# Performance work log

Measured on AMD Instinct MI355X. Metric: run time of the kernel, lower is better.

The kernel has to match this reference:

```python
import jax, jax.numpy as jnp
import numpy as np

N, M, E, H = 4096, 16384, 512, 8
D = E // H  # head dim = 64


def _rms(x, g, eps=1e-6):
    return x * jax.lax.rsqrt(jnp.mean(jnp.square(x), axis=-1, keepdims=True) + eps) * g


def _split(x):
    # (rows, E) -> (rows, H, D)
    return x.reshape(x.shape[0], H, D)


def _sdpa(q, k, v):
    # Faithful to the source layout: SDPA on (rows, H, D) tensors, i.e. per-row
    # attention over the H heads (tiny HxH softmax per node).
    s = jnp.einsum('nhd,ngd->nhg', q, k) / jnp.sqrt(jnp.asarray(D, q.dtype))
    a = jax.nn.softmax(s, axis=-1)
    return jnp.einsum('nhg,ngd->nhd', a, v).reshape(-1, E)


def setup_inputs() -> dict:
    key = jax.random.key(0)
    ks = jax.random.split(key, 25)
    w = lambda k, s, sc: jax.random.normal(k, s, dtype=jnp.float32) * sc
    se = 1.0 / np.sqrt(E)   # Linear(E, E) init scale
    sm = 1.0 / np.sqrt(M)   # Linear(M, N) init scale
    inp = {
        'x_node': jax.random.normal(ks[0], (N, E), dtype=jnp.float32),
        'x_edge': jax.random.normal(ks[1], (M, E), dtype=jnp.float32),
        # sparse-ish binary adjacency, avg degree ~8
        'adj': (jax.random.uniform(ks[2], (N, N)) < 0.002).astype(jnp.float32),
        # per-branch QKV weights (4 separate MultiHeadAttention modules)
        'Wq_hh': w(ks[3], (E, E), se), 'Wk_hh': w(ks[4], (E, E), se), 'Wv_hh': w(ks[5], (E, E), se),
        'Wq_ee': w(ks[6], (E, E), se), 'Wk_ee': w(ks[7], (E, E), se), 'Wv_ee': w(ks[8], (E, E), se),
        'Wq_he': w(ks[9], (E, E), se), 'Wk_he': w(ks[10], (E, E), se), 'Wv_he': w(ks[11], (E, E), se),
        'Wq_eh': w(ks[12], (E, E), se), 'Wk_eh': w(ks[13], (E, E), se), 'Wv_eh': w(ks[14], (E, E), se),
        # shape_proj (edges -> nodes) weights, one per module that uses it
        'Wp1_he': w(ks[15], (N, M), sm),
        'Wp1_eh': w(ks[16], (N, M), sm),
        'Wp1_ee': w(ks[17], (N, M), sm),
        # RMSNorm gains
        'g_n': jnp.ones((E,), jnp.float32),
        'g_e': jnp.ones((E,), jnp.float32),
        'g2': jnp.ones((E,), jnp.float32),
        # FeedForward
        'Wf1': w(ks[18], (E, 4 * E), se), 'bf1': jnp.zeros((4 * E,), jnp.float32),
        'Wf2': w(ks[19], (4 * E, E), 1.0 / np.sqrt(4 * E)), 'bf2': jnp.zeros((E,), jnp.float32),
    }
    return inp


def reference(x_node, x_edge, adj,
              Wq_hh, Wk_hh, Wv_hh, Wq_ee, Wk_ee, Wv_ee,
              Wq_he, Wk_he, Wv_he, Wq_eh, Wk_eh, Wv_eh,
              Wp1_he, Wp1_eh, Wp1_ee,
              g_n, g_e, g2, Wf1, bf1, Wf2, bf2):
    h = _rms(x_node, g_n)   # (N, E)
    e = _rms(x_edge, g_e)   # (M, E)

    # hh: adjacency injected into the node query branch
    q = jnp.einsum('nm,mhd->nhd', adj, _split(h @ Wq_hh))
    out_hh = _sdpa(q, _split(h @ Wk_hh), _split(h @ Wv_hh))

    # ee: edge queries/keys projected to node rows via shape_proj
    q = jnp.einsum('nm,mhd->nhd', Wp1_ee, _split(e @ Wq_ee))
    k = jnp.einsum('nm,mhd->nhd', Wp1_ee, _split(e @ Wk_ee))
    out_ee = _sdpa(q, k, _split(h @ Wv_ee))

    # eh: edge query projected to node rows, node key
    q = jnp.einsum('nm,mhd->nhd', Wp1_eh, _split(e @ Wq_eh))
    out_eh = _sdpa(q, _split(h @ Wk_eh), _split(h @ Wv_eh))

    # he: node query, edge key projected to node rows
    k = jnp.einsum('nm,mhd->nhd', Wp1_he, _split(e @ Wk_he))
    out_he = _sdpa(_split(h @ Wq_he), k, _split(h @ Wv_he))

    x = out_hh + out_ee + out_eh + out_he          # (N, E)
    y = _rms(x, g2)
    return jax.nn.gelu(y @ Wf1 + bf1, approximate=False) @ Wf2 + bf2
```

## Files before the change

### kernel.cpp

```cpp
#include <hip/hip_runtime.h>
#include <cstdint>


typedef unsigned short u16;
typedef __bf16 bf16x8 __attribute__((ext_vector_type(8)));
typedef float f32x4 __attribute__((ext_vector_type(4)));

__device__ __forceinline__ u16 f2bf(float f) {
    unsigned u = __float_as_uint(f);
    return (u16)((u + 0x7fffu + ((u >> 16) & 1u)) >> 16);
}
__device__ __forceinline__ float bf2f(u16 u) { return __uint_as_float(((unsigned)u) << 16); }
__device__ __forceinline__ float gelu_exact(float x) {
    return 0.5f * x * (1.0f + erff(x * 0.70710678118654752f));
}

__device__ __forceinline__ void gload_lds16(const void* g, void* l) {
    __builtin_amdgcn_global_load_lds(
        (const __attribute__((address_space(1))) unsigned int*)(uintptr_t)g,
        (__attribute__((address_space(3))) unsigned int*)(unsigned int)(uintptr_t)l,
        16, 0, 0);
}

__device__ __forceinline__ void swz_block(int& bx, int& by, int& bz) {
    const int nx = gridDim.x, ny = gridDim.y;
    const int nwg = nx * ny * gridDim.z;
    int lin = blockIdx.x + nx * (blockIdx.y + ny * blockIdx.z);
    const int chunk = nwg >> 3;
    lin = (lin & 7) * chunk + (lin >> 3);
    bx = lin % nx;
    lin /= nx;
    by = lin % ny;
    bz = lin / ny;
}

template <bool SWZ>
__global__ __launch_bounds__(256) void cvt_f32_bf16(const float* __restrict__ in,
                                                    u16* __restrict__ out, size_t n8) {
    size_t i = (size_t)blockIdx.x * 256 + threadIdx.x;
    size_t stride = (size_t)gridDim.x * 256;
    for (; i < n8; i += stride) {
        float4 a = ((const float4*)in)[i * 2];
        float4 b = ((const float4*)in)[i * 2 + 1];
        u16 r[8] = {f2bf(a.x), f2bf(a.y), f2bf(a.z), f2bf(a.w),
                    f2bf(b.x), f2bf(b.y), f2bf(b.z), f2bf(b.w)};
        size_t o = i;
        if constexpr (SWZ) o = (i & ~(size_t)63) | ((i & 63) ^ ((i >> 7) & 3));
        ((uint4*)out)[o] = *(const uint4*)r;
    }
}

__global__ __launch_bounds__(256) void transpose_cvt(const float* __restrict__ in,
                                                     u16* __restrict__ out, int R, int C) {
    __shared__ float tile[32][33];
    int c0 = blockIdx.x * 32, r0 = blockIdx.y * 32;
    int tx = threadIdx.x & 31, ty = threadIdx.x >> 5;
#pragma unroll
    for (int i = 0; i < 4; ++i)
        tile[ty + i * 8][tx] = in[(size_t)(r0 + ty + i * 8) * C + c0 + tx];
    __syncthreads();
#pragma unroll
    for (int i = 0; i < 4; ++i) {
        int orow = c0 + ty + i * 8;
        out[(size_t)orow * R + ((r0 + tx) ^ (((orow >> 1) & 3) << 3))] = f2bf(tile[tx][ty + i * 8]);
    }
}

struct W12 { const float* in[12]; u16* out[12]; };
__global__ __launch_bounds__(256) void transpose_cvt12(W12 w) {
    __shared__ float tile[32][33];
    const float* in = w.in[blockIdx.z];
    u16* out = w.out[blockIdx.z];
    int c0 = blockIdx.x * 32, r0 = blockIdx.y * 32;
    int tx = threadIdx.x & 31, ty = threadIdx.x >> 5;
#pragma unroll
    for (int i = 0; i < 4; ++i)
        tile[ty + i * 8][tx] = in[(size_t)(r0 + ty + i * 8) * 512 + c0 + tx];
    __syncthreads();
#pragma unroll
    for (int i = 0; i < 4; ++i) {
        int orow = c0 + ty + i * 8;
        out[(size_t)orow * 512 + ((r0 + tx) ^ (((orow >> 1) & 3) << 3))] = f2bf(tile[tx][ty + i * 8]);
    }
}

__global__ __launch_bounds__(256) void transpose_u16(const u16* __restrict__ in,
                                                     u16* __restrict__ out, int R, int C) {
    __shared__ u16 tile[32][34];
    int c0 = blockIdx.x * 32, r0 = blockIdx.y * 32;
    int tx = threadIdx.x & 31, ty = threadIdx.x >> 5;
#pragma unroll
    for (int i = 0; i < 4; ++i)
        tile[ty + i * 8][tx] = in[(size_t)(r0 + ty + i * 8) * C + c0 + tx];
    __syncthreads();
#pragma unroll
    for (int i = 0; i < 4; ++i) {
        int orow = c0 + ty + i * 8;
        out[(size_t)orow * R + ((r0 + tx) ^ (((orow >> 1) & 3) << 3))] = tile[tx][ty + i * 8];
    }
}

template <bool SWZ>
__global__ __launch_bounds__(256) void rmsnorm_bf16(const float* __restrict__ x,
                                                    const float* __restrict__ g,
                                                    u16* __restrict__ out) {
    int row = blockIdx.x, tid = threadIdx.x;
    const float* xr = x + (size_t)row * 512;
    float2 v = *(const float2*)(xr + tid * 2);
    float ss = v.x * v.x + v.y * v.y;
#pragma unroll
    for (int o = 32; o; o >>= 1) ss += __shfl_down(ss, o);
    __shared__ float red[4];
    if ((tid & 63) == 0) red[tid >> 6] = ss;
    __syncthreads();
    float tot = red[0] + red[1] + red[2] + red[3];
    float rs = rsqrtf(tot * (1.0f / 512.0f) + 1e-6f);
    unsigned pack = (unsigned)f2bf(v.x * rs * g[tid * 2]) |
                    ((unsigned)f2bf(v.y * rs * g[tid * 2 + 1]) << 16);
    int o32 = SWZ ? (tid ^ (((row >> 1) & 3) << 2)) : tid;
    ((unsigned*)out)[(size_t)row * 256 + o32] = pack;
}

__global__ __launch_bounds__(256) void adj_spmm(const float* __restrict__ adj,
                                                const u16* __restrict__ h,
                                                u16* __restrict__ out) {
    const int wave = threadIdx.x >> 6, lane = threadIdx.x & 63;
    const int n = blockIdx.x * 4 + wave;
    const float* arow = adj + (size_t)n * 4096;
    float acc[8] = {0.f, 0.f, 0.f, 0.f, 0.f, 0.f, 0.f, 0.f};
    for (int j = 0; j < 64; ++j) {
        float v = arow[j * 64 + lane];
        unsigned long long mask = __ballot(v != 0.0f);
        while (mask) {
            int bit = __ffsll((long long)mask) - 1;
            mask &= mask - 1;
            int m = j * 64 + bit;
            float w = __shfl(v, bit);
            int cs = (lane & ~3) | ((lane & 3) ^ ((m >> 1) & 3));
            uint4 q = *(const uint4*)(h + (size_t)m * 512 + cs * 8);
            const u16* qu = (const u16*)&q;
#pragma unroll
            for (int t = 0; t < 8; ++t) acc[t] += w * bf2f(qu[t]);
        }
    }
    int co = (lane & ~3) | ((lane & 3) ^ ((n >> 1) & 3));
    u16 r[8];
#pragma unroll
    for (int t = 0; t < 8; ++t) r[t] = f2bf(acc[t]);
    *(uint4*)(out + (size_t)n * 512 + co * 8) = *(const uint4*)r;
}

template <int MODE>
__device__ __forceinline__ void gemm_tile_body(const u16* __restrict__ A,
                                               const u16* __restrict__ Bt,
                                               int N, int K, int k_begin, int k_end,
                                               int rowStart, int colStart,
                                               void* __restrict__ C,
                                               const float* __restrict__ bias) {
    __shared__ u16 Asm[128 * 32];
    __shared__ u16 Bsm[128 * 32];
    const int tid = threadIdx.x;
    const int wave = tid >> 6, lane = tid & 63;
    const int wr = wave >> 1, wc = wave & 1;

    f32x4 acc[4][4];
#pragma unroll
    for (int m = 0; m < 4; ++m)
#pragma unroll
        for (int n = 0; n < 4; ++n) acc[m][n] = f32x4{0.f, 0.f, 0.f, 0.f};

    const int off0 = (wave * 2 + 0) * 1024 + lane * 16;
    const int off1 = (wave * 2 + 1) * 1024 + lane * 16;
    const int r0 = off0 >> 6, k0e = (off0 & 63) >> 1;
    const int r1 = off1 >> 6, k1e = (off1 & 63) >> 1;
    const size_t Arow0 = (size_t)(rowStart + r0) * K + k0e;
    const size_t Arow1 = (size_t)(rowStart + r1) * K + k1e;
    const size_t Brow0 = (size_t)(colStart + r0) * K + k0e;
    const size_t Brow1 = (size_t)(colStart + r1) * K + k1e;
    u16* As0 = &Asm[(wave * 2 + 0) * 512];
    u16* As1 = &Asm[(wave * 2 + 1) * 512];
    u16* Bs0 = &Bsm[(wave * 2 + 0) * 512];
    u16* Bs1 = &Bsm[(wave * 2 + 1) * 512];

    const int rsel = lane & 15, ksel = lane >> 4;
    const int fsw = (ksel ^ ((rsel >> 1) & 3)) << 3;

    for (int kk = k_begin; kk < k_end; kk += 32) {
        gload_lds16(A + Arow0 + kk, As0);
        gload_lds16(A + Arow1 + kk, As1);
        gload_lds16(Bt + Brow0 + kk, Bs0);
        gload_lds16(Bt + Brow1 + kk, Bs1);
        __syncthreads();
        bf16x8 aF[4], bF[4];
#pragma unroll
        for (int m = 0; m < 4; ++m)
            aF[m] = *(const bf16x8*)&Asm[(wr * 64 + m * 16 + rsel) * 32 + fsw];
#pragma unroll
        for (int n = 0; n < 4; ++n)
            bF[n] = *(const bf16x8*)&Bsm[(wc * 64 + n * 16 + rsel) * 32 + fsw];
#pragma unroll
        for (int m = 0; m < 4; ++m)
#pragma unroll
            for (int n = 0; n < 4; ++n)
                acc[m][n] = __builtin_amdgcn_mfma_f32_16x16x32_bf16(aF[m], bF[n], acc[m][n], 0, 0, 0);
        __syncthreads();
    }

    const int cq = (lane >> 4) * 4, cr = lane & 15;
#pragma unroll
    for (int m = 0; m < 4; ++m) {
#pragma unroll
        for (int n = 0; n < 4; ++n) {
            int col = colStart + wc * 64 + n * 16 + cr;
#pragma unroll
            for (int j = 0; j < 4; ++j) {
                int row = rowStart + wr * 64 + m * 16 + cq + j;
                float v = acc[m][n][j];
                if constexpr (MODE == 0) {
                    ((u16*)C)[(size_t)row * N + col] = f2bf(v);
                } else if constexpr (MODE == 1) {
                    v = gelu_exact(v + bias[col]);
                    ((u16*)C)[(size_t)row * N + (col ^ (((row >> 1) & 3) << 3))] = f2bf(v);
                } else {
                    if (bias) v += bias[col];
                    atomicAdd(&((float*)C)[(size_t)row * N + col], v);
                }
            }
        }
    }
}

template <int MODE>
__global__ __launch_bounds__(256) void gemm_bt(const u16* __restrict__ A,
                                               const u16* __restrict__ Bt,
                                               void* __restrict__ C,
                                               const float* __restrict__ bias,
                                               int N, int K, int kLen) {
    int bx, by, bz;
    swz_block(bx, by, bz);
    const float* bb = (MODE == 3) ? ((bz == 0) ? bias : nullptr) : bias;
    int kb = bz * kLen;
    gemm_tile_body<MODE>(A, Bt, N, K, kb, kb + kLen, by * 128, bx * 128, C, bb);
}

struct Small12 { const u16* A[12]; const u16* W[12]; u16* C[12]; };
__global__ __launch_bounds__(256) void gemm_small12(Small12 s) {
    int bx, by, bz;
    swz_block(bx, by, bz);
    gemm_tile_body<0>(s.A[bz], s.W[bz], 512, 512, 0, 512, by * 128, bx * 128, s.C[bz], nullptr);
}

struct Big3 { const float* A[3]; };
__global__ __launch_bounds__(256, 2) void gemm_f32a(Big3 ba, const u16* __restrict__ Bt,
                                                    float* __restrict__ C0, int K,
                                                    int zPerMat, int kLen) {
    __shared__ float Afs[2][4096];
    __shared__ u16 Bsm[2][4096];
    int bx, by, bz;
    swz_block(bx, by, bz);
    const int mat = bz / zPerMat, ks = bz - mat * zPerMat;
    const float* __restrict__ A = ba.A[mat];
    float* __restrict__ C = C0 + (size_t)mat * (4096 * 512);
    const int rowStart = by * 128, colStart = bx * 128;
    const int k0 = ks * kLen;

    const int tid = threadIdx.x;
    const int wave = tid >> 6, lane = tid & 63;
    const int wr = wave >> 1, wc = wave & 1;

    f32x4 acc[4][4];
#pragma unroll
    for (int mm = 0; mm < 4; ++mm)
#pragma unroll
        for (int n = 0; n < 4; ++n) acc[mm][n] = f32x4{0.f, 0.f, 0.f, 0.f};

    const int lrow = lane >> 3;
    const int slot = (lane & 7) ^ lrow;
    size_t asrc[4];
    int adst[4];
#pragma unroll
    for (int i = 0; i < 4; ++i) {
        int row = wave * 32 + i * 8 + lrow;
        asrc[i] = (size_t)(rowStart + row) * K + slot * 4;
        adst[i] = (wave * 4 + i) * 256 + lane * 4;
    }

    const int off0 = (wave * 2 + 0) * 1024 + lane * 16;
    const int off1 = (wave * 2 + 1) * 1024 + lane * 16;
    const int br0 = off0 >> 6, bk0 = (off0 & 63) >> 1;
    const int br1 = off1 >> 6, bk1 = (off1 & 63) >> 1;
    const u16* Bp0 = Bt + (size_t)(colStart + br0) * K + bk0;
    const u16* Bp1 = Bt + (size_t)(colStart + br1) * K + bk1;
    const int ws0 = (wave * 2 + 0) * 512, ws1 = (wave * 2 + 1) * 512;

    const int rsel = lane & 15, ksel = lane >> 4;
    const int fsw = (ksel ^ ((rsel >> 1) & 3)) << 3;

    auto STAGE = [&](int buf, int kk) {
#pragma unroll
        for (int i = 0; i < 4; ++i)
            gload_lds16(A + asrc[i] + kk, &Afs[buf][adst[i]]);
        gload_lds16(Bp0 + kk, &Bsm[buf][ws0]);
        gload_lds16(Bp1 + kk, &Bsm[buf][ws1]);
    };
    auto COMPUTE = [&](int buf) {
        bf16x8 aF[4], bF[4];
#pragma unroll
        for (int mm = 0; mm < 4; ++mm) {
            int R = wr * 64 + mm * 16 + rsel;
            const char* rb = (const char*)&Afs[buf][0] + R * 128;
            f32x4 lo = *(const f32x4*)(rb + ((((ksel << 1) | 0) ^ (R & 7)) << 4));
            f32x4 hi = *(const f32x4*)(rb + ((((ksel << 1) | 1) ^ (R & 7)) << 4));
            aF[mm][0] = (__bf16)lo[0]; aF[mm][1] = (__bf16)lo[1];
            aF[mm][2] = (__bf16)lo[2]; aF[mm][3] = (__bf16)lo[3];
            aF[mm][4] = (__bf16)hi[0]; aF[mm][5] = (__bf16)hi[1];
            aF[mm][6] = (__bf16)hi[2]; aF[mm][7] = (__bf16)hi[3];
        }
#pragma unroll
        for (int n = 0; n < 4; ++n)
            bF[n] = *(const bf16x8*)&Bsm[buf][(wc * 64 + n * 16 + rsel) * 32 + fsw];
#pragma unroll
        for (int mm = 0; mm < 4; ++mm)
#pragma unroll
            for (int n = 0; n < 4; ++n)
                acc[mm][n] = __builtin_amdgcn_mfma_f32_16x16x32_bf16(aF[mm], bF[n], acc[mm][n], 0, 0, 0);
    };

    const int nt = kLen >> 5;
    STAGE(0, k0);
    asm volatile("s_waitcnt vmcnt(0)");
    __builtin_amdgcn_sched_barrier(0);
    __builtin_amdgcn_s_barrier();
    __builtin_amdgcn_sched_barrier(0);

    int cur = 0;
    for (int t = 0; t < nt - 1; ++t) {
        STAGE(cur ^ 1, k0 + (t + 1) * 32);
        __builtin_amdgcn_sched_barrier(0);
        asm volatile("s_waitcnt vmcnt(6)");
        __builtin_amdgcn_sched_barrier(0);
        __builtin_amdgcn_s_barrier();
        __builtin_amdgcn_sched_barrier(0);
        COMPUTE(cur);
        __builtin_amdgcn_sched_barrier(0);
        __builtin_amdgcn_s_barrier();
        __builtin_amdgcn_sched_barrier(0);
        cur ^= 1;
    }
    asm volatile("s_waitcnt vmcnt(0)");
    __builtin_amdgcn_sched_barrier(0);
    __builtin_amdgcn_s_barrier();
    __builtin_amdgcn_sched_barrier(0);
    COMPUTE(cur);

    const int cq = (lane >> 4) * 4, cr = lane & 15;
#pragma unroll
    for (int mm = 0; mm < 4; ++mm)
#pragma unroll
        for (int n = 0; n < 4; ++n) {
            int col = colStart + wc * 64 + n * 16 + cr;
#pragma unroll
            for (int j = 0; j < 4; ++j) {
                int row = rowStart + wr * 64 + mm * 16 + cq + j;
                atomicAdd(&C[(size_t)row * 512 + col], acc[mm][n][j]);
            }
        }
}

struct SP12 { const u16* p[12]; };
__global__ __launch_bounds__(256) void sdpa_fused(SP12 sp, const float* __restrict__ g2,
                                                  u16* __restrict__ y) {
    __shared__ float qb[4][8][65], kb[4][8][65], vb[4][8][65];
    __shared__ float aw[4][64];
    __shared__ float red[4];
    const int n = blockIdx.x, tid = threadIdx.x;
    const size_t base = (size_t)n * 512;
    const int e0 = tid * 2, hs = e0 >> 6, ds = e0 & 63;

#pragma unroll
    for (int br = 0; br < 4; ++br) {
        unsigned u;
        u = *(const unsigned*)(sp.p[br * 3 + 0] + base + e0);
        qb[br][hs][ds] = bf2f(u & 0xffffu); qb[br][hs][ds + 1] = bf2f(u >> 16);
        u = *(const unsigned*)(sp.p[br * 3 + 1] + base + e0);
        kb[br][hs][ds] = bf2f(u & 0xffffu); kb[br][hs][ds + 1] = bf2f(u >> 16);
        u = *(const unsigned*)(sp.p[br * 3 + 2] + base + e0);
        vb[br][hs][ds] = bf2f(u & 0xffffu); vb[br][hs][ds + 1] = bf2f(u >> 16);
    }
    __syncthreads();

    const int b = tid >> 6, h = (tid >> 3) & 7, g = tid & 7;
    float s = 0.f;
    const float* qr = &qb[b][h][0];
    const float* kr = &kb[b][g][0];
#pragma unroll
    for (int j = 0; j < 64; ++j) s += qr[j] * kr[j];
    s *= 0.125f;
    float mx = s;
#pragma unroll
    for (int o = 1; o < 8; o <<= 1) mx = fmaxf(mx, __shfl_xor(mx, o));
    float p = expf(s - mx);
    float sm = p;
#pragma unroll
    for (int o = 1; o < 8; o <<= 1) sm += __shfl_xor(sm, o);
    aw[b][(h << 3) | g] = p / sm;
    __syncthreads();

    float o0 = 0.f, o1 = 0.f;
#pragma unroll
    for (int bb = 0; bb < 4; ++bb)
#pragma unroll
        for (int gg = 0; gg < 8; ++gg) {
            float a = aw[bb][(hs << 3) | gg];
            o0 += a * vb[bb][gg][ds];
            o1 += a * vb[bb][gg][ds + 1];
        }

    float ss = o0 * o0 + o1 * o1;
#pragma unroll
    for (int o = 32; o; o >>= 1) ss += __shfl_down(ss, o);
    if ((tid & 63) == 0) red[tid >> 6] = ss;
    __syncthreads();
    float tot = red[0] + red[1] + red[2] + red[3];
    float rs = rsqrtf(tot * (1.0f / 512.0f) + 1e-6f);
    unsigned pack = (unsigned)f2bf(o0 * rs * g2[e0]) | ((unsigned)f2bf(o1 * rs * g2[e0 + 1]) << 16);
    ((unsigned*)y)[(size_t)n * 256 + (tid ^ (((n >> 1) & 3) << 2))] = pack;
}

extern "C" void kernel_launch(void* const* d_in, const int* in_sizes, int n_in,
                              void* d_out, int out_size, void* d_ws, size_t ws_size,
                              hipStream_t stream) {
    (void)in_sizes; (void)n_in; (void)out_size; (void)ws_size;
    const int N = 4096, M = 16384, E = 512;

    const float* x_node = (const float*)d_in[0];
    const float* x_edge = (const float*)d_in[1];
    const float* adj    = (const float*)d_in[2];
    const float* Wp1_he = (const float*)d_in[15];
    const float* Wp1_eh = (const float*)d_in[16];
    const float* Wp1_ee = (const float*)d_in[17];
    const float* g_n = (const float*)d_in[18];
    const float* g_e = (const float*)d_in[19];
    const float* g2  = (const float*)d_in[20];
    const float* Wf1 = (const float*)d_in[21];
    const float* bf1 = (const float*)d_in[22];
    const float* Wf2 = (const float*)d_in[23];
    const float* bf2 = (const float*)d_in[24];

    char* p = (char*)d_ws;
    auto alloc = [&](size_t b) { char* r = p; p += (b + 255) & ~(size_t)255; return r; };
    const size_t NP = (size_t)N * E;
    const size_t WSZ = (size_t)E * E;
    u16* h    = (u16*)alloc(NP * 2);
    u16* e    = (u16*)alloc((size_t)M * E * 2);
    u16* eT   = (u16*)alloc((size_t)M * E * 2);
    u16* Wt   = (u16*)alloc(12 * WSZ * 2);
    u16* Wf1T = (u16*)alloc((size_t)2048 * 512 * 2);
    u16* Wf2T = (u16*)alloc((size_t)512 * 2048 * 2);
    float* F3 = (float*)alloc(3 * NP * 4);
    u16* P3b  = (u16*)alloc(3 * NP * 2);
    u16* Ahb  = (u16*)alloc(NP * 2);
    u16* S12  = (u16*)alloc(12 * NP * 2);
    u16* y    = (u16*)alloc(NP * 2);
    u16* t    = (u16*)alloc((size_t)N * 2048 * 2);

    W12 w12;
    for (int i = 0; i < 12; ++i) { w12.in[i] = (const float*)d_in[3 + i]; w12.out[i] = Wt + i * WSZ; }
    transpose_cvt12<<<dim3(16, 16, 12), 256, 0, stream>>>(w12);
    transpose_cvt<<<dim3(64, 16), 256, 0, stream>>>(Wf1, Wf1T, 512, 2048);
    transpose_cvt<<<dim3(16, 64), 256, 0, stream>>>(Wf2, Wf2T, 2048, 512);

    rmsnorm_bf16<true><<<N, 256, 0, stream>>>(x_node, g_n, h);
    rmsnorm_bf16<false><<<M, 256, 0, stream>>>(x_edge, g_e, e);
    transpose_u16<<<dim3(16, 512), 256, 0, stream>>>(e, eT, M, 512);
    adj_spmm<<<1024, 256, 0, stream>>>(adj, h, Ahb);

    hipMemsetAsync(F3, 0, 3 * NP * 4, stream);
    Big3 bp; bp.A[0] = Wp1_ee; bp.A[1] = Wp1_eh; bp.A[2] = Wp1_he;
    gemm_f32a<<<dim3(4, 32, 12), 256, 0, stream>>>(bp, eT, F3, M, 4, 4096);
    cvt_f32_bf16<true><<<2048, 256, 0, stream>>>(F3, P3b, 3 * NP / 8);
    const u16* Peeb = P3b + 0 * NP;
    const u16* Pehb = P3b + 1 * NP;
    const u16* Pheb = P3b + 2 * NP;

    Small12 sb;
    const u16* aList[12] = {Ahb, h, h, Peeb, Peeb, h, Pehb, h, h, h, Pheb, h};
    const int wList[12]  = {0, 1, 2, 3, 4, 5, 9, 10, 11, 6, 7, 8};
    for (int i = 0; i < 12; ++i) {
        sb.A[i] = aList[i];
        sb.W[i] = Wt + wList[i] * WSZ;
        sb.C[i] = S12 + i * NP;
    }
    gemm_small12<<<dim3(4, 32, 12), 256, 0, stream>>>(sb);

    SP12 sp;
    for (int i = 0; i < 12; ++i) sp.p[i] = S12 + i * NP;
    sdpa_fused<<<N, 256, 0, stream>>>(sp, g2, y);

    gemm_bt<1><<<dim3(16, 32, 1), 256, 0, stream>>>(y, Wf1T, t, bf1, 2048, 512, 512);
    hipMemsetAsync(d_out, 0, NP * 4, stream);
    gemm_bt<3><<<dim3(4, 32, 2), 256, 0, stream>>>(t, Wf2T, d_out, bf2, 512, 2048, 1024);
}
```

Baseline: 624.0 us.

## Triple-buffer f32-A GEMM pipeline and remap block indices for L2 locality

Moves the big shape-projection GEMM from double to triple buffering in LDS. Two tiles are now in flight ahead of compute, with a vmcnt(12) wait and a 3-way unrolled loop hard-coded for kLen=4096. The launch becomes a 1D grid with a custom block-to-tile mapping that groups blocks by XCD so they share the A rows. This should hide more global-load latency and improve cache reuse, but the extra LDS (72KB per block) may cut occupancy below the requested 2 blocks per CU. It also hard-codes the K split.

```diff
diff --git a/kernel.cpp b/kernel.cpp
--- a/kernel.cpp
+++ b/kernel.cpp
@@ -21,6 +21,8 @@
         (__attribute__((address_space(3))) unsigned int*)(unsigned int)(uintptr_t)l,
         16, 0, 0);
 }
+
+#define SCHED0 __builtin_amdgcn_sched_barrier(0)
 
 __device__ __forceinline__ void swz_block(int& bx, int& by, int& bz) {
     const int nx = gridDim.x, ny = gridDim.y;
@@ -252,16 +254,19 @@
 
 struct Big3 { const float* A[3]; };
 __global__ __launch_bounds__(256, 2) void gemm_f32a(Big3 ba, const u16* __restrict__ Bt,
-                                                    float* __restrict__ C0, int K,
-                                                    int zPerMat, int kLen) {
-    __shared__ float Afs[2][4096];
-    __shared__ u16 Bsm[2][4096];
-    int bx, by, bz;
-    swz_block(bx, by, bz);
-    const int mat = bz / zPerMat, ks = bz - mat * zPerMat;
+                                                    float* __restrict__ C0, int K) {
+    __shared__ float Afs[3][4096];
+    __shared__ u16 Bsm[3][4096];
+    const int i = blockIdx.x;
+    const int x = i & 7, j = i >> 3;
+    const int bx = j & 3;
+    const int g = x * 48 + (j >> 2);
+    const int by = g & 31, bz = g >> 5;
+    const int mat = bz >> 2, ks = bz & 3;
     const float* __restrict__ A = ba.A[mat];
     float* __restrict__ C = C0 + (size_t)mat * (4096 * 512);
     const int rowStart = by * 128, colStart = bx * 128;
+    const int kLen = 4096;
     const int k0 = ks * kLen;
 
     const int tid = threadIdx.x;
@@ -279,10 +284,10 @@
     size_t asrc[4];
     int adst[4];
 #pragma unroll
-    for (int i = 0; i < 4; ++i) {
-        int row = wave * 32 + i * 8 + lrow;
-        asrc[i] = (size_t)(rowStart + row) * K + slot * 4;
-        adst[i] = (wave * 4 + i) * 256 + lane * 4;
+    for (int ii = 0; ii < 4; ++ii) {
+        int row = wave * 32 + ii * 8 + lrow;
+        asrc[ii] = (size_t)(rowStart + row) * K + slot * 4;
+        adst[ii] = (wave * 4 + ii) * 256 + lane * 4;
     }
 
     const int off0 = (wave * 2 + 0) * 1024 + lane * 16;
@@ -298,8 +303,8 @@
 
     auto STAGE = [&](int buf, int kk) {
 #pragma unroll
-        for (int i = 0; i < 4; ++i)
-            gload_lds16(A + asrc[i] + kk, &Afs[buf][adst[i]]);
+        for (int ii = 0; ii < 4; ++ii)
+            gload_lds16(A + asrc[ii] + kk, &Afs[buf][adst[ii]]);
         gload_lds16(Bp0 + kk, &Bsm[buf][ws0]);
         gload_lds16(Bp1 + kk, &Bsm[buf][ws1]);
     };
@@ -325,33 +330,43 @@
             for (int n = 0; n < 4; ++n)
                 acc[mm][n] = __builtin_amdgcn_mfma_f32_16x16x32_bf16(aF[mm], bF[n], acc[mm][n], 0, 0, 0);
     };
-
-    const int nt = kLen >> 5;
+    auto STEP = [&](int sbuf, int cbuf, int kk) {
+        STAGE(sbuf, kk);
+        SCHED0;
+        asm volatile("s_waitcnt vmcnt(12)");
+        SCHED0;
+        __builtin_amdgcn_s_barrier();
+        SCHED0;
+        COMPUTE(cbuf);
+        SCHED0;
+        __builtin_amdgcn_s_barrier();
+        SCHED0;
+    };
+
     STAGE(0, k0);
+    STAGE(1, k0 + 32);
+    SCHED0;
+
+    int kk = k0 + 64;
+    for (int it = 0; it < 42; ++it) {
+        STEP(2, 0, kk);
+        STEP(0, 1, kk + 32);
+        STEP(1, 2, kk + 64);
+        kk += 96;
+    }
+    asm volatile("s_waitcnt vmcnt(6)");
+    SCHED0;
+    __builtin_amdgcn_s_barrier();
+    SCHED0;
+    COMPUTE(0);
+    SCHED0;
+    __builtin_amdgcn_s_barrier();
+    SCHED0;
     asm volatile("s_waitcnt vmcnt(0)");
-    __builtin_amdgcn_sched_barrier(0);
+    SCHED0;
     __builtin_amdgcn_s_barrier();
-    __builtin_amdgcn_sched_barrier(0);
-
-    int cur = 0;
-    for (int t = 0; t < nt - 1; ++t) {
-        STAGE(cur ^ 1, k0 + (t + 1) * 32);
-        __builtin_amdgcn_sched_barrier(0);
-        asm volatile("s_waitcnt vmcnt(6)");
-        __builtin_amdgcn_sched_barrier(0);
-        __builtin_amdgcn_s_barrier();
-        __builtin_amdgcn_sched_barrier(0);
-        COMPUTE(cur);
-        __builtin_amdgcn_sched_barrier(0);
-        __builtin_amdgcn_s_barrier();
-        __builtin_amdgcn_sched_barrier(0);
-        cur ^= 1;
-    }
-    asm volatile("s_waitcnt vmcnt(0)");
-    __builtin_amdgcn_sched_barrier(0);
-    __builtin_amdgcn_s_barrier();
-    __builtin_amdgcn_sched_barrier(0);
-    COMPUTE(cur);
+    SCHED0;
+    COMPUTE(1);
 
     const int cq = (lane >> 4) * 4, cr = lane & 15;
 #pragma unroll
@@ -360,9 +375,9 @@
         for (int n = 0; n < 4; ++n) {
             int col = colStart + wc * 64 + n * 16 + cr;
 #pragma unroll
-            for (int j = 0; j < 4; ++j) {
-                int row = rowStart + wr * 64 + mm * 16 + cq + j;
-                atomicAdd(&C[(size_t)row * 512 + col], acc[mm][n][j]);
+            for (int jj = 0; jj < 4; ++jj) {
+                int row = rowStart + wr * 64 + mm * 16 + cq + jj;
+                atomicAdd(&C[(size_t)row * 512 + col], acc[mm][n][jj]);
             }
         }
 }
@@ -477,7 +492,7 @@
 
     hipMemsetAsync(F3, 0, 3 * NP * 4, stream);
     Big3 bp; bp.A[0] = Wp1_ee; bp.A[1] = Wp1_eh; bp.A[2] = Wp1_he;
-    gemm_f32a<<<dim3(4, 32, 12), 256, 0, stream>>>(bp, eT, F3, M, 4, 4096);
+    gemm_f32a<<<dim3(1536), 256, 0, stream>>>(bp, eT, F3, M);
     cvt_f32_bf16<true><<<2048, 256, 0, stream>>>(F3, P3b, 3 * NP / 8);
     const u16* Peeb = P3b + 0 * NP;
     const u16* Pehb = P3b + 1 * NP;
```

Result: no change. 630.4 us (+1.0%).
